# Kernel tuning notes

Measured on AMD Instinct MI355X. Metric: run time of the kernel, lower is better.

The kernel has to match this reference:

```python
import jax, jax.numpy as jnp
import numpy as np

D_MODEL, D_STATE, D_CONV, EXPAND = 1024, 16, 4, 2
D_INNER = EXPAND * D_MODEL  # 2048
DT_RANK = (D_MODEL + 15) // 16  # 64
BATCH, SEQ = 2, 2048


def setup_inputs() -> dict:
    key = jax.random.key(0)
    ks = jax.random.split(key, 8)
    s = 0.02
    A = jnp.tile(jnp.arange(1, D_STATE + 1, dtype=jnp.float32), (D_INNER, 1))
    return {
        "x": jax.random.normal(ks[0], (BATCH, SEQ, D_MODEL), jnp.float32),
        "in_proj_w": jax.random.normal(ks[1], (D_MODEL, 2 * D_INNER), jnp.float32) * s,
        "conv_w": jax.random.normal(ks[2], (D_INNER, 1, D_CONV), jnp.float32) * s,
        "conv_b": jnp.zeros((D_INNER,), jnp.float32),
        "x_proj_w": jax.random.normal(ks[3], (D_INNER, DT_RANK + 2 * D_STATE), jnp.float32) * s,
        "dt_proj_w": jax.random.normal(ks[4], (DT_RANK, D_INNER), jnp.float32) * s,
        "dt_proj_b": jnp.zeros((D_INNER,), jnp.float32),
        "A_log": jnp.log(A),
        "D": jnp.ones((D_INNER,), jnp.float32),
        "out_proj_w": jax.random.normal(ks[5], (D_INNER, D_MODEL), jnp.float32) * s,
    }


def _mamba(x, in_proj_w, conv_w, conv_b, x_proj_w, dt_proj_w, dt_proj_b, A_log, D, out_proj_w):
    d_inner, d_state = A_log.shape
    dt_rank = dt_proj_w.shape[0]
    seq_len = x.shape[1]

    xr = x @ in_proj_w                       # (B, L, 2*ED)
    xb, res = jnp.split(xr, 2, axis=-1)      # each (B, L, ED)

    # causal depthwise conv1d (torch pads both sides then truncates to seq_len
    # == left-pad-only causal conv)
    xc = jnp.swapaxes(xb, 1, 2)              # (B, ED, L)
    xc = jax.lax.conv_general_dilated(
        xc, conv_w, window_strides=(1,),
        padding=[(conv_w.shape[-1] - 1, 0)],
        dimension_numbers=("NCH", "OIH", "NCH"),
        feature_group_count=d_inner)
    xc = xc + conv_b[None, :, None]
    u = jax.nn.silu(jnp.swapaxes(xc, 1, 2))  # (B, L, ED)

    dbc = u @ x_proj_w                       # (B, L, dt_rank + 2*N)
    dt, Bc, Cc = jnp.split(dbc, [dt_rank, dt_rank + d_state], axis=-1)
    dt = jax.nn.softplus(dt @ dt_proj_w + dt_proj_b)  # (B, L, ED)
    A = -jnp.exp(A_log)                      # (ED, N)

    def step(h, xs):
        dt_i, B_i, C_i, u_i = xs             # (B,ED), (B,N), (B,N), (B,ED)
        dA = jnp.exp(dt_i[:, :, None] * A)   # (B, ED, N)
        h = h * dA + (dt_i * u_i)[:, :, None] * B_i[:, None, :]
        y = jnp.einsum("bdn,bn->bd", h, C_i) + D * u_i
        return h, y

    h0 = jnp.zeros((x.shape[0], d_inner, d_state), x.dtype)
    xs = (jnp.swapaxes(dt, 0, 1), jnp.swapaxes(Bc, 0, 1),
          jnp.swapaxes(Cc, 0, 1), jnp.swapaxes(u, 0, 1))
    _, ys = jax.lax.scan(step, h0, xs)       # ys: (L, B, ED)
    y_ssm = jnp.swapaxes(ys, 0, 1)           # (B, L, ED)

    y = y_ssm * jax.nn.silu(res)
    return y @ out_proj_w                    # (B, L, d_model)


def reference(x, in_proj_w, conv_w, conv_b, x_proj_w, dt_proj_w, dt_proj_b, A_log, D, out_proj_w):
    return _mamba(x, in_proj_w, conv_w, conv_b, x_proj_w, dt_proj_w, dt_proj_b, A_log, D, out_proj_w)
```

## Files before the change

kernel.cpp:

```cpp
#include <hip/hip_runtime.h>
#include <cstddef>
#include <cstdint>

#define BATCH 2
#define SEQ   2048
#define DM    1024
#define ED    2048
#define NS    16
#define DR    64
#define NROWS (BATCH*SEQ)

#define NCHUNK 64
#define CLEN   32
#define CSTATES (BATCH*ED*NS)

#define OFF_XB    ((size_t)0)
#define OFF_RESH  ((size_t)8388608)
#define OFF_PS    ((size_t)12582912)
#define OFF_DT    ((size_t)20971520)
#define OFF_DBC   ((size_t)29360128)
#define OFF_PART  ((size_t)29753344)

typedef _Float16 half8 __attribute__((ext_vector_type(8)));
typedef _Float16 half4 __attribute__((ext_vector_type(4)));
typedef float    floatx4 __attribute__((ext_vector_type(4)));

__device__ __forceinline__ float silu_f(float x) { return x / (1.f + __expf(-x)); }

__device__ __forceinline__ void gload_lds16(const _Float16* g, _Float16* l) {
  __builtin_amdgcn_global_load_lds(
      (const __attribute__((address_space(1))) void*)g,
      (__attribute__((address_space(3))) void*)l, 16, 0, 0);
}

template<int BN, int WGM, int WGN, int EPI, int KSPLIT>
__global__ __launch_bounds__(256)
void hgemm(const _Float16* __restrict__ A, int lda,
           const _Float16* __restrict__ Bt, int ldb,
           const float* __restrict__ bias,
           float* __restrict__ C, _Float16* __restrict__ Ch,
           size_t cslice, int N, int K) {
  constexpr int BM = 128;
  constexpr int FM = BM / 16 / WGM;
  constexpr int FN = BN / 16 / WGN;
  __shared__ _Float16 sA[BM * 32];
  __shared__ _Float16 sB[BN * 32];
  const int tid = threadIdx.x;
  const int ln  = tid & 63;
  const int wid = tid >> 6;
  const int wm  = wid % WGM;
  const int wn  = wid / WGM;
  const int m0  = blockIdx.y * BM;
  const int n0  = blockIdx.x * BN;
  const int l15 = ln & 15;
  const int q   = ln >> 4;

  const int kLen = K / KSPLIT;
  const int kbeg = blockIdx.z * kLen;
  if (KSPLIT > 1) C += (size_t)blockIdx.z * cslice;

  floatx4 acc[FM][FN];
  #pragma unroll
  for (int i = 0; i < FM; ++i)
    #pragma unroll
    for (int j = 0; j < FN; ++j)
      acc[i][j] = floatx4{0.f, 0.f, 0.f, 0.f};

  for (int k0 = kbeg; k0 < kbeg + kLen; k0 += 32) {
    __syncthreads();
    #pragma unroll
    for (int s = 0; s < (BM * 4 + 255) / 256; ++s) {
      const int i = s * 256 + tid;
      if (BM * 4 % 256 == 0 || i < BM * 4) {
        const int m = i >> 2;
        const int cg = (i & 3) ^ ((m >> 1) & 3);
        gload_lds16(A + (size_t)(m0 + m) * lda + k0 + cg * 8, sA + i * 8);
      }
    }
    #pragma unroll
    for (int s = 0; s < (BN * 4 + 255) / 256; ++s) {
      const int i = s * 256 + tid;
      if (BN * 4 % 256 == 0 || i < BN * 4) {
        const int n = i >> 2;
        const int cg = (i & 3) ^ ((n >> 1) & 3);
        gload_lds16(Bt + (size_t)(n0 + n) * ldb + k0 + cg * 8, sB + i * 8);
      }
    }
    __syncthreads();

    half8 af[FM], bf[FN];
    #pragma unroll
    for (int fm = 0; fm < FM; ++fm) {
      const int mr = wm * FM * 16 + fm * 16 + l15;
      const int cl = q ^ ((mr >> 1) & 3);
      af[fm] = *(const half8*)(sA + mr * 32 + cl * 8);
    }
    #pragma unroll
    for (int fn = 0; fn < FN; ++fn) {
      const int nr = wn * FN * 16 + fn * 16 + l15;
      const int cl = q ^ ((nr >> 1) & 3);
      bf[fn] = *(const half8*)(sB + nr * 32 + cl * 8);
    }
    #pragma unroll
    for (int fm = 0; fm < FM; ++fm)
      #pragma unroll
      for (int fn = 0; fn < FN; ++fn)
        acc[fm][fn] = __builtin_amdgcn_mfma_f32_16x16x32_f16(
            af[fm], bf[fn], acc[fm][fn], 0, 0, 0);
  }

  #pragma unroll
  for (int fm = 0; fm < FM; ++fm) {
    #pragma unroll
    for (int fn = 0; fn < FN; ++fn) {
      const int col = n0 + wn * FN * 16 + fn * 16 + l15;
      #pragma unroll
      for (int r = 0; r < 4; ++r) {
        const int row = m0 + wm * FM * 16 + fm * 16 + q * 4 + r;
        float v = acc[fm][fn][r];
        if (EPI == 2) {
          if (col < ED) C[(size_t)row * ED + col] = v;
          else          Ch[(size_t)row * ED + (col - ED)] = (_Float16)silu_f(v);
        } else if (EPI == 3) {
          v += bias[col];
          v = fmaxf(v, 0.f) + log1pf(__expf(-fabsf(v)));
          C[(size_t)row * N + col] = v;
        } else {
          C[(size_t)row * N + col] = v;
        }
      }
    }
  }
}

__device__ __forceinline__ void transpose_tile(const float* __restrict__ src,
                                               _Float16* __restrict__ dst,
                                               int R, int C, int bx, int by,
                                               int tid) {
  __shared__ float t[32][33];
  const int tx = tid & 31, ty = tid >> 5;
  const int c0 = bx * 32, r0 = by * 32;
  #pragma unroll
  for (int s = 0; s < 4; ++s)
    t[ty + s * 8][tx] = src[(size_t)(r0 + ty + s * 8) * C + c0 + tx];
  __syncthreads();
  #pragma unroll
  for (int s = 0; s < 4; ++s)
    dst[(size_t)(c0 + ty + s * 8) * R + r0 + tx] = (_Float16)t[tx][ty + s * 8];
}

#define PREP_BLOCKS 10560
__global__ __launch_bounds__(256)
void prep_kernel(const float* __restrict__ x, _Float16* __restrict__ x_h,
                 const float* __restrict__ Win, _Float16* __restrict__ Wint,
                 const float* __restrict__ Wout, _Float16* __restrict__ Woutt,
                 const float* __restrict__ Wx, _Float16* __restrict__ Wxt,
                 const float* __restrict__ Wdt, _Float16* __restrict__ Wdtt) {
  const int bid = blockIdx.x, tid = threadIdx.x;
  if (bid < 4096) {
    const int i = bid * 1024 + tid * 4;
    const float4 v = *(const float4*)(x + i);
    half4 o;
    o[0] = (_Float16)v.x; o[1] = (_Float16)v.y;
    o[2] = (_Float16)v.z; o[3] = (_Float16)v.w;
    *(half4*)(x_h + i) = o;
  } else if (bid < 8192) {
    const int t = bid - 4096;
    transpose_tile(Win, Wint, DM, 2 * ED, t & 127, t >> 7, tid);
  } else if (bid < 10240) {
    const int t = bid - 8192;
    transpose_tile(Wout, Woutt, ED, DM, t & 31, t >> 5, tid);
  } else if (bid < 10432) {
    const int t = bid - 10240;
    transpose_tile(Wx, Wxt, ED, 96, t % 3, t / 3, tid);
  } else {
    const int t = bid - 10432;
    transpose_tile(Wdt, Wdtt, DR, ED, t & 63, t >> 6, tid);
  }
}

__global__ __launch_bounds__(256)
void conv_silu_kernel(const float* __restrict__ xb, const float* __restrict__ w,
                      const float* __restrict__ cb, _Float16* __restrict__ u_h) {
  const int idx = blockIdx.x * 256 + threadIdx.x;
  const int d = idx & (ED - 1);
  const int t = (idx >> 11) & (SEQ - 1);
  const float4 wv = ((const float4*)w)[d];
  const float* base = xb + (size_t)(idx >> 11) * ED + d;
  float acc = cb[d];
  acc = fmaf(wv.w, base[0], acc);
  if (t >= 1) acc = fmaf(wv.z, base[-ED], acc);
  if (t >= 2) acc = fmaf(wv.y, base[-2 * ED], acc);
  if (t >= 3) acc = fmaf(wv.x, base[-3 * ED], acc);
  u_h[idx] = (_Float16)silu_f(acc);
}

__global__ __launch_bounds__(256)
void xproj_reduce(const float* __restrict__ part, float* __restrict__ dbc,
                  _Float16* __restrict__ dbc64h) {
  const int idx = blockIdx.x * 256 + threadIdx.x;
  float s = 0.f;
  #pragma unroll
  for (int r = 0; r < 8; ++r) s += part[(size_t)r * NROWS * 96 + idx];
  dbc[idx] = s;
  const int col = idx % 96;
  if (col < DR) dbc64h[(idx / 96) * DR + col] = (_Float16)s;
}

__device__ __forceinline__ void conv_init(const float* xbp, int tg0,
                                          float& x1, float& x2, float& x3) {
  x1 = (tg0 >= 1) ? xbp[-(int)ED] : 0.f;
  x2 = (tg0 >= 2) ? xbp[-2 * (int)ED] : 0.f;
  x3 = (tg0 >= 3) ? xbp[-3 * (int)ED] : 0.f;
}

__global__ __launch_bounds__(256)
void scan2_summary(const float* __restrict__ dt, const float* __restrict__ xb,
                   const float* __restrict__ convw, const float* __restrict__ convb,
                   const float* __restrict__ dbc, const float* __restrict__ A_log,
                   float* __restrict__ Pbuf, float* __restrict__ Sbuf) {
  const int d = blockIdx.x * 256 + threadIdx.x;
  const int b = blockIdx.y;
  const int g = blockIdx.z;

  float Adn[16];
  {
    const float4* al = (const float4*)(A_log + (size_t)d * NS);
    #pragma unroll
    for (int i = 0; i < 4; ++i) {
      const float4 v = al[i];
      Adn[i * 4 + 0] = -__expf(v.x); Adn[i * 4 + 1] = -__expf(v.y);
      Adn[i * 4 + 2] = -__expf(v.z); Adn[i * 4 + 3] = -__expf(v.w);
    }
  }
  const float4 wv = ((const float4*)convw)[d];
  const float cbd = convb[d];

  float P[16], S[16];
  #pragma unroll
  for (int n = 0; n < 16; ++n) { P[n] = 1.f; S[n] = 0.f; }

  const int tg0 = g * CLEN;
  const size_t row0 = (size_t)b * SEQ + tg0;
  const float* dtp = dt + row0 * ED + d;
  const float* xbp = xb + row0 * ED + d;
  float x1, x2, x3;
  conv_init(xbp, tg0, x1, x2, x3);

  for (int t = 0; t < CLEN; ++t) {
    const float xt  = xbp[(size_t)t * ED];
    const float dti = dtp[(size_t)t * ED];
    float cv = cbd;
    cv = fmaf(wv.w, xt, cv);
    cv = fmaf(wv.z, x1, cv);
    cv = fmaf(wv.y, x2, cv);
    cv = fmaf(wv.x, x3, cv);
    const float ui = silu_f(cv);
    x3 = x2; x2 = x1; x1 = xt;

    const float4* bc = (const float4*)(dbc + (row0 + t) * 96 + DR);
    float Bv[16];
    #pragma unroll
    for (int i = 0; i < 4; ++i) {
      const float4 v = bc[i];
      Bv[i * 4 + 0] = v.x; Bv[i * 4 + 1] = v.y;
      Bv[i * 4 + 2] = v.z; Bv[i * 4 + 3] = v.w;
    }
    const float dtu = dti * ui;
    #pragma unroll
    for (int n = 0; n < 16; ++n) {
      const float a = __expf(dti * Adn[n]);
      S[n] = fmaf(S[n], a, dtu * Bv[n]);
      P[n] *= a;
    }
  }
  const size_t c0 = (size_t)g * CSTATES + ((size_t)(b * ED + d)) * NS;
  #pragma unroll
  for (int i = 0; i < 4; ++i) {
    *(float4*)(Pbuf + c0 + i * 4) = float4{P[i*4], P[i*4+1], P[i*4+2], P[i*4+3]};
    *(float4*)(Sbuf + c0 + i * 4) = float4{S[i*4], S[i*4+1], S[i*4+2], S[i*4+3]};
  }
}

__global__ __launch_bounds__(256)
void scan2_compose(float* __restrict__ Pbuf, const float* __restrict__ Sbuf) {
  const unsigned c = blockIdx.x * 256 + threadIdx.x;
  float h = 0.f;
  for (int g = 0; g < NCHUNK; ++g) {
    const size_t idx = (size_t)g * CSTATES + c;
    const float p = Pbuf[idx], s = Sbuf[idx];
    Pbuf[idx] = h;
    h = fmaf(p, h, s);
  }
}

__global__ __launch_bounds__(256)
void scan2_apply(const float* __restrict__ dt, const float* __restrict__ xb,
                 const float* __restrict__ convw, const float* __restrict__ convb,
                 const float* __restrict__ dbc, const float* __restrict__ A_log,
                 const float* __restrict__ Dp, const float* __restrict__ Pbuf,
                 _Float16* __restrict__ resh) {
  const int d = blockIdx.x * 256 + threadIdx.x;
  const int b = blockIdx.y;
  const int g = blockIdx.z;

  float Adn[16];
  {
    const float4* al = (const float4*)(A_log + (size_t)d * NS);
    #pragma unroll
    for (int i = 0; i < 4; ++i) {
      const float4 v = al[i];
      Adn[i * 4 + 0] = -__expf(v.x); Adn[i * 4 + 1] = -__expf(v.y);
      Adn[i * 4 + 2] = -__expf(v.z); Adn[i * 4 + 3] = -__expf(v.w);
    }
  }
  const float4 wv = ((const float4*)convw)[d];
  const float cbd = convb[d];
  const float Dd = Dp[d];

  float h[16];
  const size_t c0 = (size_t)g * CSTATES + ((size_t)(b * ED + d)) * NS;
  #pragma unroll
  for (int i = 0; i < 4; ++i) {
    const float4 v = *(const float4*)(Pbuf + c0 + i * 4);
    h[i * 4 + 0] = v.x; h[i * 4 + 1] = v.y;
    h[i * 4 + 2] = v.z; h[i * 4 + 3] = v.w;
  }

  const int tg0 = g * CLEN;
  const size_t row0 = (size_t)b * SEQ + tg0;
  const float* dtp = dt + row0 * ED + d;
  const float* xbp = xb + row0 * ED + d;
  _Float16* rp = resh + row0 * ED + d;
  float x1, x2, x3;
  conv_init(xbp, tg0, x1, x2, x3);

  for (int t = 0; t < CLEN; ++t) {
    const float xt  = xbp[(size_t)t * ED];
    const float dti = dtp[(size_t)t * ED];
    float cv = cbd;
    cv = fmaf(wv.w, xt, cv);
    cv = fmaf(wv.z, x1, cv);
    cv = fmaf(wv.y, x2, cv);
    cv = fmaf(wv.x, x3, cv);
    const float ui = silu_f(cv);
    x3 = x2; x2 = x1; x1 = xt;

    const float4* bc = (const float4*)(dbc + (row0 + t) * 96 + DR);
    float Bv[16], Cv[16];
    #pragma unroll
    for (int i = 0; i < 4; ++i) {
      const float4 v = bc[i];
      Bv[i * 4 + 0] = v.x; Bv[i * 4 + 1] = v.y;
      Bv[i * 4 + 2] = v.z; Bv[i * 4 + 3] = v.w;
      const float4 w = bc[4 + i];
      Cv[i * 4 + 0] = w.x; Cv[i * 4 + 1] = w.y;
      Cv[i * 4 + 2] = w.z; Cv[i * 4 + 3] = w.w;
    }
    const float dtu = dti * ui;
    float y = Dd * ui;
    #pragma unroll
    for (int n = 0; n < 16; ++n) {
      const float a = __expf(dti * Adn[n]);
      h[n] = fmaf(h[n], a, dtu * Bv[n]);
      y = fmaf(h[n], Cv[n], y);
    }
    const float sres = (float)rp[(size_t)t * ED];
    rp[(size_t)t * ED] = (_Float16)(y * sres);
  }
}

extern "C" void kernel_launch(void* const* d_in, const int* in_sizes, int n_in,
                              void* d_out, int out_size, void* d_ws, size_t ws_size,
                              hipStream_t stream) {
  (void)in_sizes; (void)n_in; (void)out_size; (void)ws_size;
  const float* x     = (const float*)d_in[0];
  const float* Win   = (const float*)d_in[1];
  const float* convw = (const float*)d_in[2];
  const float* convb = (const float*)d_in[3];
  const float* Wx    = (const float*)d_in[4];
  const float* Wdt   = (const float*)d_in[5];
  const float* bdt   = (const float*)d_in[6];
  const float* Alog  = (const float*)d_in[7];
  const float* Dp    = (const float*)d_in[8];
  const float* Wout  = (const float*)d_in[9];

  float* ws   = (float*)d_ws;
  float* xb   = ws + OFF_XB;
  _Float16* resh = (_Float16*)(ws + OFF_RESH);
  float* Pbuf = ws + OFF_PS;
  float* Sbuf = ws + OFF_PS + 4194304;
  float* dt   = ws + OFF_DT;
  float* dbc  = ws + OFF_DBC;
  float* part = ws + OFF_PART;
  _Float16* Woutt  = (_Float16*)(part + 4194304);
  _Float16* Wxt    = (_Float16*)(part + 5242880);
  _Float16* dbc64h = (_Float16*)(part + 5341184);
  _Float16* Wdtt   = (_Float16*)(part + 5472256);
  float* out  = (float*)d_out;

  _Float16* x_h  = (_Float16*)(ws + OFF_DT);
  _Float16* Wint = (_Float16*)(ws + OFF_DT + 2097152);
  _Float16* u_h  = (_Float16*)(ws + OFF_DT + 4194304);

  prep_kernel<<<PREP_BLOCKS, 256, 0, stream>>>(
      x, x_h, Win, Wint, Wout, Woutt, Wx, Wxt, Wdt, Wdtt);
  hgemm<128, 2, 2, 2, 1><<<dim3((2 * ED) / 128, NROWS / 128), 256, 0, stream>>>(
      x_h, DM, Wint, DM, nullptr, xb, resh, 0, 2 * ED, DM);
  conv_silu_kernel<<<(NROWS * ED) / 256, 256, 0, stream>>>(xb, convw, convb, u_h);
  hgemm<96, 4, 1, 0, 8><<<dim3(1, NROWS / 128, 8), 256, 0, stream>>>(
      u_h, ED, Wxt, ED, nullptr, part, nullptr, (size_t)NROWS * 96, 96, ED);
  xproj_reduce<<<(NROWS * 96) / 256, 256, 0, stream>>>(part, dbc, dbc64h);
  hgemm<128, 2, 2, 3, 1><<<dim3(ED / 128, NROWS / 128), 256, 0, stream>>>(
      dbc64h, DR, Wdtt, DR, bdt, dt, nullptr, 0, ED, DR);
  scan2_summary<<<dim3(ED / 256, BATCH, NCHUNK), 256, 0, stream>>>(
      dt, xb, convw, convb, dbc, Alog, Pbuf, Sbuf);
  scan2_compose<<<CSTATES / 256, 256, 0, stream>>>(Pbuf, Sbuf);
  scan2_apply<<<dim3(ED / 256, BATCH, NCHUNK), 256, 0, stream>>>(
      dt, xb, convw, convb, dbc, Alog, Dp, Pbuf, resh);
  hgemm<64, 4, 1, 0, 1><<<dim3(DM / 64, NROWS / 128), 256, 0, stream>>>(
      resh, ED, Woutt, ED, nullptr, out, nullptr, 0, DM, ED);
}
```

Before: 364.5 us.

## Store xb and dt intermediates in fp16 and use BK=64 GEMM tiles

The in_proj GEMM now writes the xb half as fp16 and the dt_proj GEMM writes softplus(dt) as fp16. The conv and both scan kernels read these fp16 buffers and convert to float, roughly halving the memory traffic on these large intermediates. The workspace offsets are shrunk to match. Separately, the hgemm template gains a BK parameter, and all GEMMs now stage 64-wide K slices with a wider XOR swizzle. This halves the number of barriers per K loop at the cost of more LDS per block. Rounding dt and xb to fp16 adds some precision loss inside the recurrence.

```diff
diff --git a/kernel.cpp b/kernel.cpp
--- a/kernel.cpp
+++ b/kernel.cpp
@@ -14,12 +14,12 @@
 #define CLEN   32
 #define CSTATES (BATCH*ED*NS)
 
-#define OFF_XB    ((size_t)0)
-#define OFF_RESH  ((size_t)8388608)
-#define OFF_PS    ((size_t)12582912)
-#define OFF_DT    ((size_t)20971520)
-#define OFF_DBC   ((size_t)29360128)
-#define OFF_PART  ((size_t)29753344)
+#define OFF_XBH   ((size_t)0)
+#define OFF_RESH  ((size_t)4194304)
+#define OFF_PS    ((size_t)8388608)
+#define OFF_DT    ((size_t)16777216)
+#define OFF_DBC   ((size_t)25165824)
+#define OFF_PART  ((size_t)25559040)
 
 typedef _Float16 half8 __attribute__((ext_vector_type(8)));
 typedef _Float16 half4 __attribute__((ext_vector_type(4)));
@@ -33,18 +33,20 @@
       (__attribute__((address_space(3))) void*)l, 16, 0, 0);
 }
 
-template<int BN, int WGM, int WGN, int EPI, int KSPLIT>
+template<int BN, int WGM, int WGN, int EPI, int KSPLIT, int BK>
 __global__ __launch_bounds__(256)
 void hgemm(const _Float16* __restrict__ A, int lda,
            const _Float16* __restrict__ Bt, int ldb,
            const float* __restrict__ bias,
            float* __restrict__ C, _Float16* __restrict__ Ch,
+           _Float16* __restrict__ Ch2,
            size_t cslice, int N, int K) {
   constexpr int BM = 128;
   constexpr int FM = BM / 16 / WGM;
   constexpr int FN = BN / 16 / WGN;
-  __shared__ _Float16 sA[BM * 32];
-  __shared__ _Float16 sB[BN * 32];
+  constexpr int CPR = BK / 8;
+  __shared__ _Float16 sA[BM * BK];
+  __shared__ _Float16 sB[BN * BK];
   const int tid = threadIdx.x;
   const int ln  = tid & 63;
   const int wid = tid >> 6;
@@ -66,47 +68,46 @@
     for (int j = 0; j < FN; ++j)
       acc[i][j] = floatx4{0.f, 0.f, 0.f, 0.f};
 
-  for (int k0 = kbeg; k0 < kbeg + kLen; k0 += 32) {
+  for (int k0 = kbeg; k0 < kbeg + kLen; k0 += BK) {
     __syncthreads();
     #pragma unroll
-    for (int s = 0; s < (BM * 4 + 255) / 256; ++s) {
+    for (int s = 0; s < (BM * CPR) / 256; ++s) {
       const int i = s * 256 + tid;
-      if (BM * 4 % 256 == 0 || i < BM * 4) {
-        const int m = i >> 2;
-        const int cg = (i & 3) ^ ((m >> 1) & 3);
-        gload_lds16(A + (size_t)(m0 + m) * lda + k0 + cg * 8, sA + i * 8);
+      const int m = i / CPR;
+      const int cg = (i & (CPR - 1)) ^ ((m >> 1) & (CPR - 1));
+      gload_lds16(A + (size_t)(m0 + m) * lda + k0 + cg * 8, sA + i * 8);
+    }
+    #pragma unroll
+    for (int s = 0; s < (BN * CPR) / 256; ++s) {
+      const int i = s * 256 + tid;
+      const int n = i / CPR;
+      const int cg = (i & (CPR - 1)) ^ ((n >> 1) & (CPR - 1));
+      gload_lds16(Bt + (size_t)(n0 + n) * ldb + k0 + cg * 8, sB + i * 8);
+    }
+    __syncthreads();
+
+    #pragma unroll
+    for (int h = 0; h < BK / 32; ++h) {
+      half8 af[FM], bf[FN];
+      #pragma unroll
+      for (int fm = 0; fm < FM; ++fm) {
+        const int mr = wm * FM * 16 + fm * 16 + l15;
+        const int cl = (h * 4 + q) ^ ((mr >> 1) & (CPR - 1));
+        af[fm] = *(const half8*)(sA + mr * BK + cl * 8);
       }
-    }
-    #pragma unroll
-    for (int s = 0; s < (BN * 4 + 255) / 256; ++s) {
-      const int i = s * 256 + tid;
-      if (BN * 4 % 256 == 0 || i < BN * 4) {
-        const int n = i >> 2;
-        const int cg = (i & 3) ^ ((n >> 1) & 3);
-        gload_lds16(Bt + (size_t)(n0 + n) * ldb + k0 + cg * 8, sB + i * 8);
+      #pragma unroll
+      for (int fn = 0; fn < FN; ++fn) {
+        const int nr = wn * FN * 16 + fn * 16 + l15;
+        const int cl = (h * 4 + q) ^ ((nr >> 1) & (CPR - 1));
+        bf[fn] = *(const half8*)(sB + nr * BK + cl * 8);
       }
-    }
-    __syncthreads();
-
-    half8 af[FM], bf[FN];
-    #pragma unroll
-    for (int fm = 0; fm < FM; ++fm) {
-      const int mr = wm * FM * 16 + fm * 16 + l15;
-      const int cl = q ^ ((mr >> 1) & 3);
-      af[fm] = *(const half8*)(sA + mr * 32 + cl * 8);
-    }
-    #pragma unroll
-    for (int fn = 0; fn < FN; ++fn) {
-      const int nr = wn * FN * 16 + fn * 16 + l15;
-      const int cl = q ^ ((nr >> 1) & 3);
-      bf[fn] = *(const half8*)(sB + nr * 32 + cl * 8);
-    }
-    #pragma unroll
-    for (int fm = 0; fm < FM; ++fm)
       #pragma unroll
-      for (int fn = 0; fn < FN; ++fn)
-        acc[fm][fn] = __builtin_amdgcn_mfma_f32_16x16x32_f16(
-            af[fm], bf[fn], acc[fm][fn], 0, 0, 0);
+      for (int fm = 0; fm < FM; ++fm)
+        #pragma unroll
+        for (int fn = 0; fn < FN; ++fn)
+          acc[fm][fn] = __builtin_amdgcn_mfma_f32_16x16x32_f16(
+              af[fm], bf[fn], acc[fm][fn], 0, 0, 0);
+    }
   }
 
   #pragma unroll
@@ -119,12 +120,12 @@
         const int row = m0 + wm * FM * 16 + fm * 16 + q * 4 + r;
         float v = acc[fm][fn][r];
         if (EPI == 2) {
-          if (col < ED) C[(size_t)row * ED + col] = v;
-          else          Ch[(size_t)row * ED + (col - ED)] = (_Float16)silu_f(v);
+          if (col < ED) Ch[(size_t)row * ED + col] = (_Float16)v;
+          else          Ch2[(size_t)row * ED + (col - ED)] = (_Float16)silu_f(v);
         } else if (EPI == 3) {
           v += bias[col];
           v = fmaxf(v, 0.f) + log1pf(__expf(-fabsf(v)));
-          C[(size_t)row * N + col] = v;
+          Ch[(size_t)row * N + col] = (_Float16)v;
         } else {
           C[(size_t)row * N + col] = v;
         }
@@ -180,18 +181,18 @@
 }
 
 __global__ __launch_bounds__(256)
-void conv_silu_kernel(const float* __restrict__ xb, const float* __restrict__ w,
+void conv_silu_kernel(const _Float16* __restrict__ xbh, const float* __restrict__ w,
                       const float* __restrict__ cb, _Float16* __restrict__ u_h) {
   const int idx = blockIdx.x * 256 + threadIdx.x;
   const int d = idx & (ED - 1);
   const int t = (idx >> 11) & (SEQ - 1);
   const float4 wv = ((const float4*)w)[d];
-  const float* base = xb + (size_t)(idx >> 11) * ED + d;
+  const _Float16* base = xbh + (size_t)(idx >> 11) * ED + d;
   float acc = cb[d];
-  acc = fmaf(wv.w, base[0], acc);
-  if (t >= 1) acc = fmaf(wv.z, base[-ED], acc);
-  if (t >= 2) acc = fmaf(wv.y, base[-2 * ED], acc);
-  if (t >= 3) acc = fmaf(wv.x, base[-3 * ED], acc);
+  acc = fmaf(wv.w, (float)base[0], acc);
+  if (t >= 1) acc = fmaf(wv.z, (float)base[-ED], acc);
+  if (t >= 2) acc = fmaf(wv.y, (float)base[-2 * ED], acc);
+  if (t >= 3) acc = fmaf(wv.x, (float)base[-3 * ED], acc);
   u_h[idx] = (_Float16)silu_f(acc);
 }
 
@@ -207,15 +208,15 @@
   if (col < DR) dbc64h[(idx / 96) * DR + col] = (_Float16)s;
 }
 
-__device__ __forceinline__ void conv_init(const float* xbp, int tg0,
-                                          float& x1, float& x2, float& x3) {
-  x1 = (tg0 >= 1) ? xbp[-(int)ED] : 0.f;
-  x2 = (tg0 >= 2) ? xbp[-2 * (int)ED] : 0.f;
-  x3 = (tg0 >= 3) ? xbp[-3 * (int)ED] : 0.f;
-}
-
-__global__ __launch_bounds__(256)
-void scan2_summary(const float* __restrict__ dt, const float* __restrict__ xb,
+__device__ __forceinline__ void conv_init_h(const _Float16* xbp, int tg0,
+                                            float& x1, float& x2, float& x3) {
+  x1 = (tg0 >= 1) ? (float)xbp[-(int)ED] : 0.f;
+  x2 = (tg0 >= 2) ? (float)xbp[-2 * (int)ED] : 0.f;
+  x3 = (tg0 >= 3) ? (float)xbp[-3 * (int)ED] : 0.f;
+}
+
+__global__ __launch_bounds__(256)
+void scan2_summary(const _Float16* __restrict__ dth, const _Float16* __restrict__ xbh,
                    const float* __restrict__ convw, const float* __restrict__ convb,
                    const float* __restrict__ dbc, const float* __restrict__ A_log,
                    float* __restrict__ Pbuf, float* __restrict__ Sbuf) {
@@ -242,14 +243,14 @@
 
   const int tg0 = g * CLEN;
   const size_t row0 = (size_t)b * SEQ + tg0;
-  const float* dtp = dt + row0 * ED + d;
-  const float* xbp = xb + row0 * ED + d;
+  const _Float16* dtp = dth + row0 * ED + d;
+  const _Float16* xbp = xbh + row0 * ED + d;
   float x1, x2, x3;
-  conv_init(xbp, tg0, x1, x2, x3);
+  conv_init_h(xbp, tg0, x1, x2, x3);
 
   for (int t = 0; t < CLEN; ++t) {
-    const float xt  = xbp[(size_t)t * ED];
-    const float dti = dtp[(size_t)t * ED];
+    const float xt  = (float)xbp[(size_t)t * ED];
+    const float dti = (float)dtp[(size_t)t * ED];
     float cv = cbd;
     cv = fmaf(wv.w, xt, cv);
     cv = fmaf(wv.z, x1, cv);
@@ -295,7 +296,7 @@
 }
 
 __global__ __launch_bounds__(256)
-void scan2_apply(const float* __restrict__ dt, const float* __restrict__ xb,
+void scan2_apply(const _Float16* __restrict__ dth, const _Float16* __restrict__ xbh,
                  const float* __restrict__ convw, const float* __restrict__ convb,
                  const float* __restrict__ dbc, const float* __restrict__ A_log,
                  const float* __restrict__ Dp, const float* __restrict__ Pbuf,
@@ -329,15 +330,15 @@
 
   const int tg0 = g * CLEN;
   const size_t row0 = (size_t)b * SEQ + tg0;
-  const float* dtp = dt + row0 * ED + d;
-  const float* xbp = xb + row0 * ED + d;
+  const _Float16* dtp = dth + row0 * ED + d;
+  const _Float16* xbp = xbh + row0 * ED + d;
   _Float16* rp = resh + row0 * ED + d;
   float x1, x2, x3;
-  conv_init(xbp, tg0, x1, x2, x3);
+  conv_init_h(xbp, tg0, x1, x2, x3);
 
   for (int t = 0; t < CLEN; ++t) {
-    const float xt  = xbp[(size_t)t * ED];
-    const float dti = dtp[(size_t)t * ED];
+    const float xt  = (float)xbp[(size_t)t * ED];
+    const float dti = (float)dtp[(size_t)t * ED];
     float cv = cbd;
     cv = fmaf(wv.w, xt, cv);
     cv = fmaf(wv.z, x1, cv);
@@ -386,17 +387,17 @@
   const float* Wout  = (const float*)d_in[9];
 
   float* ws   = (float*)d_ws;
-  float* xb   = ws + OFF_XB;
+  _Float16* xbh  = (_Float16*)(ws + OFF_XBH);
   _Float16* resh = (_Float16*)(ws + OFF_RESH);
   float* Pbuf = ws + OFF_PS;
   float* Sbuf = ws + OFF_PS + 4194304;
-  float* dt   = ws + OFF_DT;
+  _Float16* dth = (_Float16*)(ws + OFF_DT);
   float* dbc  = ws + OFF_DBC;
   float* part = ws + OFF_PART;
-  _Float16* Woutt  = (_Float16*)(part + 4194304);
-  _Float16* Wxt    = (_Float16*)(part + 5242880);
-  _Float16* dbc64h = (_Float16*)(part + 5341184);
-  _Float16* Wdtt   = (_Float16*)(part + 5472256);
+  _Float16* Woutt  = (_Float16*)(part + 3145728);
+  _Float16* Wxt    = (_Float16*)(part + 4194304);
+  _Float16* dbc64h = (_Float16*)(part + 4292608);
+  _Float16* Wdtt   = (_Float16*)(part + 4423680);
   float* out  = (float*)d_out;
 
   _Float16* x_h  = (_Float16*)(ws + OFF_DT);
@@ -405,19 +406,19 @@
 
   prep_kernel<<<PREP_BLOCKS, 256, 0, stream>>>(
       x, x_h, Win, Wint, Wout, Woutt, Wx, Wxt, Wdt, Wdtt);
-  hgemm<128, 2, 2, 2, 1><<<dim3((2 * ED) / 128, NROWS / 128), 256, 0, stream>>>(
-      x_h, DM, Wint, DM, nullptr, xb, resh, 0, 2 * ED, DM);
-  conv_silu_kernel<<<(NROWS * ED) / 256, 256, 0, stream>>>(xb, convw, convb, u_h);
-  hgemm<96, 4, 1, 0, 8><<<dim3(1, NROWS / 128, 8), 256, 0, stream>>>(
-      u_h, ED, Wxt, ED, nullptr, part, nullptr, (size_t)NROWS * 96, 96, ED);
+  hgemm<128, 2, 2, 2, 1, 64><<<dim3((2 * ED) / 128, NROWS / 128), 256, 0, stream>>>(
+      x_h, DM, Wint, DM, nullptr, nullptr, xbh, resh, 0, 2 * ED, DM);
+  conv_silu_kernel<<<(NROWS * ED) / 256, 256, 0, stream>>>(xbh, convw, convb, u_h);
+  hgemm<96, 4, 1, 0, 8, 64><<<dim3(1, NROWS / 128, 8), 256, 0, stream>>>(
+      u_h, ED, Wxt, ED, nullptr, part, nullptr, nullptr, (size_t)NROWS * 96, 96, ED);
   xproj_reduce<<<(NROWS * 96) / 256, 256, 0, stream>>>(part, dbc, dbc64h);
-  hgemm<128, 2, 2, 3, 1><<<dim3(ED / 128, NROWS / 128), 256, 0, stream>>>(
-      dbc64h, DR, Wdtt, DR, bdt, dt, nullptr, 0, ED, DR);
+  hgemm<128, 2, 2, 3, 1, 64><<<dim3(ED / 128, NROWS / 128), 256, 0, stream>>>(
+      dbc64h, DR, Wdtt, DR, bdt, nullptr, dth, nullptr, 0, ED, DR);
   scan2_summary<<<dim3(ED / 256, BATCH, NCHUNK), 256, 0, stream>>>(
-      dt, xb, convw, convb, dbc, Alog, Pbuf, Sbuf);
+      dth, xbh, convw, convb, dbc, Alog, Pbuf, Sbuf);
   scan2_compose<<<CSTATES / 256, 256, 0, stream>>>(Pbuf, Sbuf);
   scan2_apply<<<dim3(ED / 256, BATCH, NCHUNK), 256, 0, stream>>>(
-      dt, xb, convw, convb, dbc, Alog, Dp, Pbuf, resh);
-  hgemm<64, 4, 1, 0, 1><<<dim3(DM / 64, NROWS / 128), 256, 0, stream>>>(
-      resh, ED, Woutt, ED, nullptr, out, nullptr, 0, DM, ED);
-}
+      dth, xbh, convw, convb, dbc, Alog, Dp, Pbuf, resh);
+  hgemm<64, 4, 1, 0, 1, 64><<<dim3(DM / 64, NROWS / 128), 256, 0, stream>>>(
+      resh, ED, Woutt, ED, nullptr, out, nullptr, nullptr, 0, DM, ED);
+}
```

New measurement: 351.2 us. 1.04x faster.
